# Kernel tuning notes

Hardware: AMD Instinct MI355X
Metric: run time of the kernel (lower is better)

## Reference

```python
import jax, jax.numpy as jnp
import numpy as np

B, T, C = 4, 2048, 1024
T_PAST = 2048


def setup_inputs() -> dict:
    key = jax.random.key(0)
    ks = jax.random.split(key, 9)
    s = 1.0 / np.sqrt(C)
    return {
        "x": jax.random.normal(ks[0], (B, T, C), dtype=jnp.float32),
        "past_k": jax.random.normal(ks[1], (B, T_PAST, C), dtype=jnp.float32),
        "past_v": jax.random.normal(ks[2], (B, T_PAST, C), dtype=jnp.float32),
        "Wq": jax.random.normal(ks[3], (C, C), dtype=jnp.float32) * s,
        "bq": jnp.zeros((C,), dtype=jnp.float32),
        "Wk": jax.random.normal(ks[4], (C, C), dtype=jnp.float32) * s,
        "bk": jnp.zeros((C,), dtype=jnp.float32),
        "Wv": jax.random.normal(ks[5], (C, C), dtype=jnp.float32) * s,
        "bv": jnp.zeros((C,), dtype=jnp.float32),
    }


def reference(x, past_k, past_v, Wq, bq, Wk, bk, Wv, bv):
    Bb, Tt, Cc = x.shape
    # nn.Linear: y = x @ W^T + b
    Q = jnp.einsum('btc,dc->btd', x, Wq) + bq
    K = jnp.einsum('btc,dc->btd', x, Wk) + bk
    V = jnp.einsum('btc,dc->btd', x, Wv) + bv
    K = jnp.concatenate([past_k, K], axis=1)
    V = jnp.concatenate([past_v, V], axis=1)
    T_total = K.shape[1]
    scores = jnp.einsum('btc,bsc->bts', Q, K) / jnp.sqrt(jnp.float32(Cc))
    # Faithful to torch.tril(ones(T, T_total)): allow j <= i (even across cache)
    mask = jnp.arange(T_total)[None, :] <= jnp.arange(Tt)[:, None]
    scores = jnp.where(mask[None, :, :], scores, -jnp.inf)
    weights = jax.nn.softmax(scores, axis=-1)
    out = jnp.einsum('bts,bsc->btc', weights, V)
    return (out, K, V)
```

## Files before the change

kernel.cpp:

```cpp
#include <hip/hip_runtime.h>


typedef __bf16 bf16x8 __attribute__((ext_vector_type(8)));
typedef float f32x4 __attribute__((ext_vector_type(4)));

#define BB   4
#define TQ   2048
#define CD   1024
#define TPAST 2048
#define TTOT 4096
#define MROWS (BB * TQ)
#define SSTRIDE ((size_t)TTOT * CD * 2)
#define SLOTU 8192

__device__ __forceinline__ unsigned short f32_to_bf16u(float f) {
  unsigned int u = __float_as_uint(f);
  u += 0x7FFFu + ((u >> 16) & 1u);
  return (unsigned short)(u >> 16);
}
__device__ __forceinline__ float bf16u_to_f32(unsigned short h) {
  unsigned int u = ((unsigned int)h) << 16;
  return __uint_as_float(u);
}
__device__ __forceinline__ unsigned int pack_bf16(float a, float b) {
  return (unsigned int)f32_to_bf16u(a) | ((unsigned int)f32_to_bf16u(b) << 16);
}

__device__ __forceinline__ void gload_lds16(const unsigned short* g,
                                            unsigned short* l) {
  __builtin_amdgcn_global_load_lds(
      (const __attribute__((address_space(1))) void*)g,
      (__attribute__((address_space(3))) void*)l, 16, 0, 0);
}

struct StagePtrs {
  const unsigned short *a0, *a1, *b0, *b1;
};

__device__ __forceinline__ void stage_step(StagePtrs& p, unsigned short* lds,
                                           int stOff, int wv) {
  unsigned short* base = lds + stOff + wv * 512;
  gload_lds16(p.a0, base);
  gload_lds16(p.a1, base + 2048);
  gload_lds16(p.b0, base + 4096);
  gload_lds16(p.b1, base + 6144);
  p.a0 += 32; p.a1 += 32; p.b0 += 32; p.b1 += 32;
}

__device__ __forceinline__ void gemm_core_v2(
    StagePtrs p, unsigned short* lds, int NT,
    int wr, int wc, int lane, int wv, f32x4 acc[4][4]) {
  const int gph8 = (((lane >> 4) ^ (lane & 3))) * 8;
  const int aRd = (wr * 64 + (lane & 15)) * 32 + gph8;
  const int bRd = 4096 + (wc * 64 + (lane & 15)) * 32 + gph8;

  stage_step(p, lds, 0, wv);
  stage_step(p, lds, SLOTU, wv);
  int stOff = 2 * SLOTU;
  int rdOff = 0;

  for (int t = 0; t < NT; ++t) {
    if (t + 2 < NT) {
      stage_step(p, lds, stOff, wv);
      stOff = (stOff == 2 * SLOTU) ? 0 : stOff + SLOTU;
    }
    const int rem = NT - 1 - t;
    if (rem >= 2)      asm volatile("s_waitcnt vmcnt(8)" ::: "memory");
    else if (rem == 1) asm volatile("s_waitcnt vmcnt(4)" ::: "memory");
    else               asm volatile("s_waitcnt vmcnt(0)" ::: "memory");
    asm volatile("s_barrier" ::: "memory");
    bf16x8 af[4], bg[4];
#pragma unroll
    for (int i = 0; i < 4; ++i)
      af[i] = *(const bf16x8*)&lds[rdOff + aRd + i * 512];
#pragma unroll
    for (int i = 0; i < 4; ++i)
      bg[i] = *(const bf16x8*)&lds[rdOff + bRd + i * 512];
    asm volatile("s_waitcnt lgkmcnt(0)" ::: "memory");
    __builtin_amdgcn_sched_barrier(0);
    asm volatile("s_barrier" ::: "memory");
    __builtin_amdgcn_s_setprio(1);
#pragma unroll
    for (int mi = 0; mi < 4; ++mi)
#pragma unroll
      for (int ni = 0; ni < 4; ++ni)
        acc[mi][ni] = __builtin_amdgcn_mfma_f32_16x16x32_bf16(
            af[mi], bg[ni], acc[mi][ni], 0, 0, 0);
    __builtin_amdgcn_s_setprio(0);
    rdOff = (rdOff == 2 * SLOTU) ? 0 : rdOff + SLOTU;
  }
}

__device__ __forceinline__ const unsigned short* swz_src(
    const unsigned short* base, size_t rowStart, size_t ld,
    int part, int wv, int lane) {
  int row = part * 64 + wv * 16 + (lane >> 2);
  int gp = (lane & 3) ^ ((lane >> 2) & 3);
  return base + (rowStart + row) * ld + gp * 8;
}

#define TP_PAD 134
#define VCT_BLOCKS 2048
#define R0_END 2097152
#define R1_END 2359296
#define R2_END 2621440
#define R3_END 2883584
#define R4_END 4980736
__global__ __launch_bounds__(256) void prep(
    const float* __restrict__ x, const float* __restrict__ wq,
    const float* __restrict__ wk, const float* __restrict__ wv,
    const float* __restrict__ pk, const float* __restrict__ pV,
    unsigned short* __restrict__ xb, unsigned short* __restrict__ wqb,
    unsigned short* __restrict__ wkb, unsigned short* __restrict__ wvb,
    unsigned short* __restrict__ kb,
    float* __restrict__ outV, unsigned short* __restrict__ VT) {
  const int tid = threadIdx.x;
  if (blockIdx.x < VCT_BLOCKS) {
    __shared__ unsigned short T[32 * TP_PAD];
    const int bid = blockIdx.x;
    const int s0 = (bid & 63) * 32, c0 = ((bid >> 6) & 7) * 128, b = bid >> 9;
    const int s = tid >> 3, i8 = tid & 7;
    const float* src = &pV[(size_t)(b * TPAST + s0 + s) * CD + c0];
    float* dst = &outV[(size_t)b * (TTOT * CD) + (size_t)(s0 + s) * CD + c0];
#pragma unroll
    for (int k = 0; k < 4; ++k) {
      int c = k * 32 + i8 * 4;
      float4 f = *(const float4*)&src[c];
      *(float4*)&dst[c] = f;
      *(unsigned int*)&T[s * TP_PAD + c]     = pack_bf16(f.x, f.y);
      *(unsigned int*)&T[s * TP_PAD + c + 2] = pack_bf16(f.z, f.w);
    }
    __syncthreads();
    const int c = tid >> 2, sq = tid & 3;
#pragma unroll
    for (int ii = 0; ii < 2; ++ii) {
      int cc = c + ii * 64;
      unsigned short tmp[8];
#pragma unroll
      for (int j = 0; j < 8; ++j) tmp[j] = T[(sq * 8 + j) * TP_PAD + cc];
      *(uint4*)&VT[(size_t)(b * CD + c0 + cc) * TPAST + s0 + sq * 8] = *(uint4*)tmp;
    }
    return;
  }
  int i = (blockIdx.x - VCT_BLOCKS) * 256 + tid;
  const float* src; unsigned short* dst; int off;
  if (i < R0_END)      { src = x;  dst = xb;  off = i; }
  else if (i < R1_END) { src = wq; dst = wqb; off = i - R0_END; }
  else if (i < R2_END) { src = wk; dst = wkb; off = i - R1_END; }
  else if (i < R3_END) { src = wv; dst = wvb; off = i - R2_END; }
  else                 { src = pk; dst = kb;  off = i - R3_END; }
  float4 f = ((const float4*)src)[off];
  uint2 o;
  o.x = pack_bf16(f.x, f.y);
  o.y = pack_bf16(f.z, f.w);
  ((uint2*)dst)[off] = o;
}

__global__ __launch_bounds__(256) void copy_past_kernel(
    const float* __restrict__ src, float* __restrict__ dst) {
  int i = blockIdx.x * 256 + threadIdx.x;
  int b = i >> 19;
  int rem = i & 524287;
  ((float4*)dst)[(size_t)b * 1048576 + rem] = ((const float4*)src)[i];
}

__global__ __launch_bounds__(256, 3) void proj_qkv(
    const unsigned short* __restrict__ A,
    const unsigned short* __restrict__ Wq_,
    const unsigned short* __restrict__ Wv_,
    const unsigned short* __restrict__ Wk_,
    const float* __restrict__ bq_, const float* __restrict__ bv_,
    const float* __restrict__ bk_,
    unsigned short* __restrict__ outQ,
    float* __restrict__ outV, float* __restrict__ outK) {
  __shared__ unsigned short lds[3 * SLOTU];
  const int tm = blockIdx.x * 128;
  const int which = blockIdx.y >> 3;
  const int tn = (blockIdx.y & 7) * 128;
  const unsigned short* W = (which == 0) ? Wq_ : (which == 1) ? Wv_ : Wk_;
  const float* bias = (which == 0) ? bq_ : (which == 1) ? bv_ : bk_;
  const int tid = threadIdx.x, lane = tid & 63, wv = tid >> 6;
  const int wr = wv >> 1, wc = wv & 1;
  StagePtrs p;
  p.a0 = swz_src(A, tm, CD, 0, wv, lane);
  p.a1 = swz_src(A, tm, CD, 1, wv, lane);
  p.b0 = swz_src(W, tn, CD, 0, wv, lane);
  p.b1 = swz_src(W, tn, CD, 1, wv, lane);
  f32x4 acc[4][4] = {};
  gemm_core_v2(p, lds, CD / 32, wr, wc, lane, wv, acc);
  const int rsub = (lane >> 4) * 4, csub = lane & 15;
#pragma unroll
  for (int mi = 0; mi < 4; ++mi)
#pragma unroll
    for (int ni = 0; ni < 4; ++ni) {
      int gcn = tn + wc * 64 + ni * 16 + csub;
      float bvv = bias[gcn];
#pragma unroll
      for (int r = 0; r < 4; ++r) {
        int grw = tm + wr * 64 + mi * 16 + rsub + r;
        float v = acc[mi][ni][r] + bvv;
        if (which == 0) {
          outQ[(size_t)grw * CD + gcn] = f32_to_bf16u(v * 0.03125f);
        } else {
          int b = grw >> 11, t = grw & (TQ - 1);
          float* o = (which == 1) ? outV : outK;
          o[(size_t)b * (TTOT * CD) + (size_t)(TPAST + t) * CD + gcn] = v;
        }
      }
    }
}

__global__ __launch_bounds__(256, 3) void score_gemm(
    const unsigned short* __restrict__ Q,
    const unsigned short* __restrict__ KB,
    unsigned short* __restrict__ S16) {
  const int t0 = blockIdx.x * 128, s0 = blockIdx.y * 128, b = blockIdx.z;
  if (s0 > t0 + 127) return;
  __shared__ unsigned short lds[3 * SLOTU];
  const int tid = threadIdx.x, lane = tid & 63, wv = tid >> 6;
  const int wr = wv >> 1, wc = wv & 1;
  StagePtrs p;
  p.a0 = swz_src(Q, (size_t)b * TQ + t0, CD, 0, wv, lane);
  p.a1 = swz_src(Q, (size_t)b * TQ + t0, CD, 1, wv, lane);
  p.b0 = swz_src(KB, (size_t)b * TPAST + s0, CD, 0, wv, lane);
  p.b1 = swz_src(KB, (size_t)b * TPAST + s0, CD, 1, wv, lane);
  f32x4 acc[4][4] = {};
  gemm_core_v2(p, lds, CD / 32, wr, wc, lane, wv, acc);
  const int rsub = (lane >> 4) * 4, csub = lane & 15;
#pragma unroll
  for (int mi = 0; mi < 4; ++mi)
#pragma unroll
    for (int ni = 0; ni < 4; ++ni) {
      int gs = s0 + wc * 64 + ni * 16 + csub;
#pragma unroll
      for (int r = 0; r < 4; ++r) {
        int gt = t0 + wr * 64 + mi * 16 + rsub + r;
        S16[(size_t)b * SSTRIDE + (size_t)gt * TPAST + gs] =
            f32_to_bf16u(acc[mi][ni][r]);
      }
    }
}

__global__ __launch_bounds__(256) void softmax_kernel(unsigned short* __restrict__ S16) {
  const int row = blockIdx.x;
  const int b = row >> 11, t = row & (TQ - 1);
  unsigned short* p = S16 + (size_t)b * SSTRIDE + (size_t)t * TPAST;
  const int tid = threadIdx.x, lane = tid & 63, wv = tid >> 6;
  __shared__ float red[8];
  const int base = tid * 8;
  uint4 raw = *(const uint4*)&p[base];
  const unsigned short* rw = (const unsigned short*)&raw;
  float v[8];
  float m = -3.0e38f;
#pragma unroll
  for (int i = 0; i < 8; ++i) {
    v[i] = (base + i <= t) ? bf16u_to_f32(rw[i]) : -3.0e38f;
    m = fmaxf(m, v[i]);
  }
#pragma unroll
  for (int off = 32; off >= 1; off >>= 1) m = fmaxf(m, __shfl_down(m, off));
  if (lane == 0) red[wv] = m;
  __syncthreads();
  if (tid == 0) red[4] = fmaxf(fmaxf(red[0], red[1]), fmaxf(red[2], red[3]));
  __syncthreads();
  const float rm = red[4];
  float e[8], s = 0.f;
#pragma unroll
  for (int i = 0; i < 8; ++i) {
    e[i] = (base + i <= t) ? __expf(v[i] - rm) : 0.f;
    s += e[i];
  }
#pragma unroll
  for (int off = 32; off >= 1; off >>= 1) s += __shfl_down(s, off);
  __syncthreads();
  if (lane == 0) red[wv] = s;
  __syncthreads();
  if (tid == 0) red[5] = red[0] + red[1] + red[2] + red[3];
  __syncthreads();
  const float inv = 1.f / red[5];
  unsigned short ob[8];
#pragma unroll
  for (int i = 0; i < 8; ++i) ob[i] = f32_to_bf16u(e[i] * inv);
  *(uint4*)&p[base] = *(uint4*)ob;
}

__global__ __launch_bounds__(256, 3) void pv_gemm(
    const unsigned short* __restrict__ Pb,
    const unsigned short* __restrict__ VT,
    float* __restrict__ O) {
  const int t0 = blockIdx.x * 128, c0 = blockIdx.y * 128, b = blockIdx.z;
  __shared__ unsigned short lds[3 * SLOTU];
  const int tid = threadIdx.x, lane = tid & 63, wv = tid >> 6;
  const int wr = wv >> 1, wc = wv & 1;
  StagePtrs p;
  p.a0 = swz_src(Pb + (size_t)b * SSTRIDE, t0, TPAST, 0, wv, lane);
  p.a1 = swz_src(Pb + (size_t)b * SSTRIDE, t0, TPAST, 1, wv, lane);
  p.b0 = swz_src(VT, (size_t)b * CD + c0, TPAST, 0, wv, lane);
  p.b1 = swz_src(VT, (size_t)b * CD + c0, TPAST, 1, wv, lane);
  f32x4 acc[4][4] = {};
  const int s_end = (t0 + 128 < TPAST) ? (t0 + 128) : TPAST;
  gemm_core_v2(p, lds, s_end / 32, wr, wc, lane, wv, acc);
  const int rsub = (lane >> 4) * 4, csub = lane & 15;
#pragma unroll
  for (int mi = 0; mi < 4; ++mi)
#pragma unroll
    for (int ni = 0; ni < 4; ++ni) {
      int gcn = c0 + wc * 64 + ni * 16 + csub;
#pragma unroll
      for (int r = 0; r < 4; ++r) {
        int gt = t0 + wr * 64 + mi * 16 + rsub + r;
        O[(size_t)(b * TQ + gt) * CD + gcn] = acc[mi][ni][r];
      }
    }
}

extern "C" void kernel_launch(void* const* d_in, const int* in_sizes, int n_in,
                              void* d_out, int out_size, void* d_ws, size_t ws_size,
                              hipStream_t stream) {
  const float* x  = (const float*)d_in[0];
  const float* pk = (const float*)d_in[1];
  const float* pv = (const float*)d_in[2];
  const float* Wq = (const float*)d_in[3];
  const float* bq = (const float*)d_in[4];
  const float* Wk = (const float*)d_in[5];
  const float* bk = (const float*)d_in[6];
  const float* Wv = (const float*)d_in[7];
  const float* bv = (const float*)d_in[8];

  float* out  = (float*)d_out;
  float* outK = out + (size_t)BB * TQ * CD;
  float* outV = outK + (size_t)BB * TTOT * CD;
  unsigned short* S16 = (unsigned short*)outK;

  unsigned short* xb  = (unsigned short*)d_ws;
  unsigned short* wqb = xb + (size_t)MROWS * CD;
  unsigned short* wkb = wqb + (size_t)CD * CD;
  unsigned short* wvb = wkb + (size_t)CD * CD;
  unsigned short* qb  = wvb + (size_t)CD * CD;
  unsigned short* vtb = qb + (size_t)MROWS * CD;
  unsigned short* kb  = vtb + (size_t)BB * CD * TPAST;

  prep<<<VCT_BLOCKS + R4_END / 256, 256, 0, stream>>>(
      x, Wq, Wk, Wv, pk, pv, xb, wqb, wkb, wvb, kb, outV, vtb);
  proj_qkv<<<dim3(MROWS / 128, 24), 256, 0, stream>>>(
      xb, wqb, wvb, wkb, bq, bv, bk, qb, outV, outK);
  score_gemm<<<dim3(TQ / 128, TPAST / 128, BB), 256, 0, stream>>>(qb, kb, S16);
  softmax_kernel<<<BB * TQ, 256, 0, stream>>>(S16);
  pv_gemm<<<dim3(TQ / 128, CD / 128, BB), 256, 0, stream>>>(S16, vtb, out);
  copy_past_kernel<<<BB * TPAST * CD / 4 / 256, 256, 0, stream>>>(pk, outK);
}
```

Before: 215.8 us.

## Use 256x256 eight-wave GEMM tiles for QKV projection and score kernels

Adds a new GEMM core that uses 256x256 output tiles with 512 threads (8 waves), each wave computing a 128x64 sub-tile. It also raises wave priority around the MFMA block. The QKV projection and score GEMM move to this core to raise arithmetic intensity and cut global and LDS traffic per FLOP. In exchange, the new LDS staging drops the XOR swizzle, so reads may hit bank conflicts. The 96KB LDS footprint limits occupancy, and the causal score grid shrinks to far fewer, coarser blocks, which can leave compute units idle and waste work on diagonal tiles.

```diff
diff --git a/kernel.cpp b/kernel.cpp
--- a/kernel.cpp
+++ b/kernel.cpp
@@ -12,6 +12,7 @@
 #define MROWS (BB * TQ)
 #define SSTRIDE ((size_t)TTOT * CD * 2)
 #define SLOTU 8192
+#define V3_SLOT 16384
 
 __device__ __forceinline__ unsigned short f32_to_bf16u(float f) {
   unsigned int u = __float_as_uint(f);
@@ -33,9 +34,73 @@
       (__attribute__((address_space(3))) void*)l, 16, 0, 0);
 }
 
-struct StagePtrs {
-  const unsigned short *a0, *a1, *b0, *b1;
-};
+struct Stage3 { const unsigned short *a0, *a1, *b0, *b1; };
+
+__device__ __forceinline__ Stage3 mk3(const unsigned short* A, size_t aRow,
+                                      size_t lda, const unsigned short* B,
+                                      size_t bRow, size_t ldb, int wv, int lane) {
+  Stage3 p;
+  const size_t r = wv * 16 + (lane >> 2);
+  const size_t c = (size_t)(lane & 3) * 8;
+  p.a0 = A + (aRow + r) * lda + c;
+  p.a1 = A + (aRow + 128 + r) * lda + c;
+  p.b0 = B + (bRow + r) * ldb + c;
+  p.b1 = B + (bRow + 128 + r) * ldb + c;
+  return p;
+}
+
+__device__ __forceinline__ void stage3(Stage3& p, unsigned short* lds,
+                                       int off, int wv) {
+  unsigned short* d = lds + off + wv * 512;
+  gload_lds16(p.a0, d);
+  gload_lds16(p.a1, d + 4096);
+  gload_lds16(p.b0, d + 8192);
+  gload_lds16(p.b1, d + 12288);
+  p.a0 += 32; p.a1 += 32; p.b0 += 32; p.b1 += 32;
+}
+
+__device__ __forceinline__ void gemm_core_v3(
+    Stage3 p, unsigned short* lds, int NT, int wm, int wn, int lane, int wv,
+    f32x4 acc[8][4]) {
+  const int koff = (lane >> 4) * 8;
+  const int aRd = (wm * 128 + (lane & 15)) * 32 + koff;
+  const int bRd = 8192 + (wn * 64 + (lane & 15)) * 32 + koff;
+  stage3(p, lds, 0, wv);
+  stage3(p, lds, V3_SLOT, wv);
+  int stOff = 2 * V3_SLOT, rdOff = 0;
+  for (int t = 0; t < NT; ++t) {
+    if (t + 2 < NT) {
+      stage3(p, lds, stOff, wv);
+      stOff = (stOff == 2 * V3_SLOT) ? 0 : stOff + V3_SLOT;
+    }
+    const int rem = NT - 1 - t;
+    if (rem >= 2)      asm volatile("s_waitcnt vmcnt(8)" ::: "memory");
+    else if (rem == 1) asm volatile("s_waitcnt vmcnt(4)" ::: "memory");
+    else               asm volatile("s_waitcnt vmcnt(0)" ::: "memory");
+    asm volatile("s_barrier" ::: "memory");
+    bf16x8 af[8], bg[4];
+#pragma unroll
+    for (int i = 0; i < 8; ++i)
+      af[i] = *(const bf16x8*)&lds[rdOff + aRd + i * 512];
+#pragma unroll
+    for (int i = 0; i < 4; ++i)
+      bg[i] = *(const bf16x8*)&lds[rdOff + bRd + i * 512];
+    asm volatile("s_waitcnt lgkmcnt(0)" ::: "memory");
+    __builtin_amdgcn_sched_barrier(0);
+    asm volatile("s_barrier" ::: "memory");
+    __builtin_amdgcn_s_setprio(1);
+#pragma unroll
+    for (int mi = 0; mi < 8; ++mi)
+#pragma unroll
+      for (int ni = 0; ni < 4; ++ni)
+        acc[mi][ni] = __builtin_amdgcn_mfma_f32_16x16x32_bf16(
+            af[mi], bg[ni], acc[mi][ni], 0, 0, 0);
+    __builtin_amdgcn_s_setprio(0);
+    rdOff = (rdOff == 2 * V3_SLOT) ? 0 : rdOff + V3_SLOT;
+  }
+}
+
+struct StagePtrs { const unsigned short *a0, *a1, *b0, *b1; };
 
 __device__ __forceinline__ void stage_step(StagePtrs& p, unsigned short* lds,
                                            int stOff, int wv) {
@@ -53,12 +118,10 @@
   const int gph8 = (((lane >> 4) ^ (lane & 3))) * 8;
   const int aRd = (wr * 64 + (lane & 15)) * 32 + gph8;
   const int bRd = 4096 + (wc * 64 + (lane & 15)) * 32 + gph8;
-
   stage_step(p, lds, 0, wv);
   stage_step(p, lds, SLOTU, wv);
   int stOff = 2 * SLOTU;
   int rdOff = 0;
-
   for (int t = 0; t < NT; ++t) {
     if (t + 2 < NT) {
       stage_step(p, lds, stOff, wv);
@@ -164,7 +227,7 @@
   ((float4*)dst)[(size_t)b * 1048576 + rem] = ((const float4*)src)[i];
 }
 
-__global__ __launch_bounds__(256, 3) void proj_qkv(
+__global__ __launch_bounds__(512, 2) void proj_qkv(
     const unsigned short* __restrict__ A,
     const unsigned short* __restrict__ Wq_,
     const unsigned short* __restrict__ Wv_,
@@ -173,31 +236,27 @@
     const float* __restrict__ bk_,
     unsigned short* __restrict__ outQ,
     float* __restrict__ outV, float* __restrict__ outK) {
-  __shared__ unsigned short lds[3 * SLOTU];
-  const int tm = blockIdx.x * 128;
-  const int which = blockIdx.y >> 3;
-  const int tn = (blockIdx.y & 7) * 128;
+  __shared__ unsigned short lds[3 * V3_SLOT];
+  const int tm = blockIdx.x * 256;
+  const int which = blockIdx.y >> 2;
+  const int tn = (blockIdx.y & 3) * 256;
   const unsigned short* W = (which == 0) ? Wq_ : (which == 1) ? Wv_ : Wk_;
   const float* bias = (which == 0) ? bq_ : (which == 1) ? bv_ : bk_;
   const int tid = threadIdx.x, lane = tid & 63, wv = tid >> 6;
-  const int wr = wv >> 1, wc = wv & 1;
-  StagePtrs p;
-  p.a0 = swz_src(A, tm, CD, 0, wv, lane);
-  p.a1 = swz_src(A, tm, CD, 1, wv, lane);
-  p.b0 = swz_src(W, tn, CD, 0, wv, lane);
-  p.b1 = swz_src(W, tn, CD, 1, wv, lane);
-  f32x4 acc[4][4] = {};
-  gemm_core_v2(p, lds, CD / 32, wr, wc, lane, wv, acc);
+  const int wm = wv >> 2, wn = wv & 3;
+  Stage3 p = mk3(A, tm, CD, W, tn, CD, wv, lane);
+  f32x4 acc[8][4] = {};
+  gemm_core_v3(p, lds, CD / 32, wm, wn, lane, wv, acc);
   const int rsub = (lane >> 4) * 4, csub = lane & 15;
 #pragma unroll
-  for (int mi = 0; mi < 4; ++mi)
+  for (int mi = 0; mi < 8; ++mi)
 #pragma unroll
     for (int ni = 0; ni < 4; ++ni) {
-      int gcn = tn + wc * 64 + ni * 16 + csub;
+      int gcn = tn + wn * 64 + ni * 16 + csub;
       float bvv = bias[gcn];
 #pragma unroll
       for (int r = 0; r < 4; ++r) {
-        int grw = tm + wr * 64 + mi * 16 + rsub + r;
+        int grw = tm + wm * 128 + mi * 16 + rsub + r;
         float v = acc[mi][ni][r] + bvv;
         if (which == 0) {
           outQ[(size_t)grw * CD + gcn] = f32_to_bf16u(v * 0.03125f);
@@ -210,31 +269,28 @@
     }
 }
 
-__global__ __launch_bounds__(256, 3) void score_gemm(
+__global__ __launch_bounds__(512, 2) void score_gemm(
     const unsigned short* __restrict__ Q,
     const unsigned short* __restrict__ KB,
     unsigned short* __restrict__ S16) {
-  const int t0 = blockIdx.x * 128, s0 = blockIdx.y * 128, b = blockIdx.z;
-  if (s0 > t0 + 127) return;
-  __shared__ unsigned short lds[3 * SLOTU];
+  const int t0 = blockIdx.x * 256, s0 = blockIdx.y * 256, b = blockIdx.z;
+  if (s0 > t0) return;
+  __shared__ unsigned short lds[3 * V3_SLOT];
   const int tid = threadIdx.x, lane = tid & 63, wv = tid >> 6;
-  const int wr = wv >> 1, wc = wv & 1;
-  StagePtrs p;
-  p.a0 = swz_src(Q, (size_t)b * TQ + t0, CD, 0, wv, lane);
-  p.a1 = swz_src(Q, (size_t)b * TQ + t0, CD, 1, wv, lane);
-  p.b0 = swz_src(KB, (size_t)b * TPAST + s0, CD, 0, wv, lane);
-  p.b1 = swz_src(KB, (size_t)b * TPAST + s0, CD, 1, wv, lane);
-  f32x4 acc[4][4] = {};
-  gemm_core_v2(p, lds, CD / 32, wr, wc, lane, wv, acc);
+  const int wm = wv >> 2, wn = wv & 3;
+  Stage3 p = mk3(Q, (size_t)b * TQ + t0, CD,
+                 KB, (size_t)b * TPAST + s0, CD, wv, lane);
+  f32x4 acc[8][4] = {};
+  gemm_core_v3(p, lds, CD / 32, wm, wn, lane, wv, acc);
   const int rsub = (lane >> 4) * 4, csub = lane & 15;
 #pragma unroll
-  for (int mi = 0; mi < 4; ++mi)
+  for (int mi = 0; mi < 8; ++mi)
 #pragma unroll
     for (int ni = 0; ni < 4; ++ni) {
-      int gs = s0 + wc * 64 + ni * 16 + csub;
+      int gs = s0 + wn * 64 + ni * 16 + csub;
 #pragma unroll
       for (int r = 0; r < 4; ++r) {
-        int gt = t0 + wr * 64 + mi * 16 + rsub + r;
+        int gt = t0 + wm * 128 + mi * 16 + rsub + r;
         S16[(size_t)b * SSTRIDE + (size_t)gt * TPAST + gs] =
             f32_to_bf16u(acc[mi][ni][r]);
       }
@@ -342,9 +398,9 @@
 
   prep<<<VCT_BLOCKS + R4_END / 256, 256, 0, stream>>>(
       x, Wq, Wk, Wv, pk, pv, xb, wqb, wkb, wvb, kb, outV, vtb);
-  proj_qkv<<<dim3(MROWS / 128, 24), 256, 0, stream>>>(
+  proj_qkv<<<dim3(MROWS / 256, 12), 512, 0, stream>>>(
       xb, wqb, wvb, wkb, bq, bv, bk, qb, outV, outK);
-  score_gemm<<<dim3(TQ / 128, TPAST / 128, BB), 256, 0, stream>>>(qb, kb, S16);
+  score_gemm<<<dim3(TQ / 256, TPAST / 256, BB), 512, 0, stream>>>(qb, kb, S16);
   softmax_kernel<<<BB * TQ, 256, 0, stream>>>(S16);
   pv_gemm<<<dim3(TQ / 128, CD / 128, BB), 256, 0, stream>>>(S16, vtb, out);
   copy_past_kernel<<<BB * TPAST * CD / 4 / 256, 256, 0, stream>>>(pk, outK);
```

New measurement: 234.8 us. +8.8%, slower.
